# Kernel optimization log

Measured on AMD Instinct MI355X. Metric: run time of the kernel, lower is better.

## Reference

```python
import jax, jax.numpy as jnp
import numpy as np

K1, K2, ALPHA = 0.01, 0.03, 0.84
SIGMA_LEVELS = (1, 2, 4, 7)

def _box_conv(x, k):
    # x: [B,1,H,W]; uniform k x k mean filter, padding k//2 (matches F.conv2d)
    p = k // 2
    w = jnp.ones((1, 1, k, k), x.dtype) / (k * k)
    return jax.lax.conv_general_dilated(
        x, w, window_strides=(1, 1), padding=((p, p), (p, p)),
        dimension_numbers=('NCHW', 'OIHW', 'NCHW'))

def _ssim_mean(X, Y, C1, C2, k):
    ux = _box_conv(X, k)
    uy = _box_conv(Y, k)
    uxx = _box_conv(X * X, k)
    uyy = _box_conv(Y * Y, k)
    uxy = _box_conv(X * Y, k)
    vx = uxx - ux * ux
    vy = uyy - uy * uy
    vxy = uxy - ux * uy
    A1 = 2 * ux * uy + C1
    A2 = 2 * vxy + C2
    B1 = ux * ux + uy * uy + C1
    B2 = vx + vy + C2
    S = (A1 * A2) / (B1 * B2)
    return jnp.mean(S)

def setup_inputs() -> dict:
    key = jax.random.key(0)
    k1, k2 = jax.random.split(key)
    B, H, W = 128, 384, 384
    X = jax.random.uniform(k1, (B, H, W), dtype=jnp.float32)
    Y = jax.random.uniform(k2, (B, H, W), dtype=jnp.float32)
    data_range = jnp.ones((B,), dtype=jnp.float32)
    return {"X": X, "Y": Y, "data_range": data_range}

def reference(X, Y, data_range):
    X4 = X[:, None, :, :]   # [B,1,H,W]
    Y4 = Y[:, None, :, :]
    dr = data_range[:, None, None, None]  # [B,1,1,1]
    C1 = (K1 * dr) ** 2
    C2 = (K2 * dr) ** 2
    # msssim = product of scalar SSIM means over sigma levels (ones_like * scalars).mean()
    msssim = jnp.float32(1.0)
    for k in SIGMA_LEVELS:
        msssim = msssim * _ssim_mean(X4, Y4, C1, C2, k)
    msssim_loss = 1.0 - msssim
    kM = SIGMA_LEVELS[-1]
    fX = _box_conv(X4, kM)
    fY = _box_conv(Y4, kM)
    l1 = jnp.mean(jnp.abs(fX - fY))
    return ALPHA * msssim_loss + (1.0 - ALPHA) * l1
```

## Files before the change

kernel.cpp:

```cpp
#include <hip/hip_runtime.h>


#define W 384
#define H 384
#define NB 128
#define BAND 48
#define NSTRIPS 4
#define NBLK (NSTRIPS * 2 * NB)

typedef __attribute__((ext_vector_type(2))) float f2;

__device__ __forceinline__ float bp(int addr, float v) {
    return __int_as_float(__builtin_amdgcn_ds_bpermute(addr, __float_as_int(v)));
}

__device__ __forceinline__ f2 f2s(float v) { f2 r; r.x = v; r.y = v; return r; }

__device__ __forceinline__ f2 ssim_pm2(f2 Vp, f2 Vm, f2 Vpp, f2 Vmm,
                                       float k2, float c1k42, float c2k42) {
    const f2 p2 = Vp * Vp;
    const f2 m2 = Vm * Vm;
    const f2 d  = p2 - m2;
    const f2 s  = p2 + m2;
    const f2 dq = Vpp - Vmm;
    const f2 sq = Vpp + Vmm;
    const f2 A1 = d + c1k42;
    const f2 B1 = s + c1k42;
    const f2 A2 = __builtin_elementwise_fma(f2s(k2), dq, -d) + c2k42;
    const f2 B2 = __builtin_elementwise_fma(f2s(k2), sq, -s) + c2k42;
    const f2 num = A1 * A2;
    const f2 den = B1 * B2;
    f2 r;
    r.x = num.x * __builtin_amdgcn_rcpf(den.x);
    r.y = num.y * __builtin_amdgcn_rcpf(den.y);
    return r;
}

__global__ __launch_bounds__(256) void msssim_main(
    const float* __restrict__ X, const float* __restrict__ Y,
    const float* __restrict__ dr, float* __restrict__ part)
{
    const int lane = threadIdx.x & 63;
    const int wv   = threadIdx.x >> 6;
    const int strip= blockIdx.x;
    const int band = blockIdx.y * 4 + wv;
    const int b    = blockIdx.z;

    const int i0 = 112 * strip - 4 + 2 * lane;
    const int i1 = i0 + 1;
    const int R0 = BAND * band;

    const int g1hi  = R0 + 48;
    const int g24hi = (band == 7) ? 385 : R0 + 48;

    const float drb = dr[b];
    const float C1 = (0.01f * drb) * (0.01f * drb);
    const float C2 = (0.03f * drb) * (0.03f * drb);
    const float tC1 = 2.f * C1;
    const float C1_2 = C1 * 32.f,    C2_2 = C2 * 32.f;
    const float C1_4 = C1 * 512.f,   C2_4 = C2 * 512.f;
    const float C1_7 = C1 * 4802.f,  C2_7 = C2 * 4802.f;

    const int lo   = 112 * strip;
    const int hi17 = (lo + 112 < 384) ? lo + 112 : 384;
    const int hi24 = (lo + 112 < 385) ? lo + 112 : 385;
    auto own = [&](int j, int hi) -> float {
        return (j >= lo && j < hi) ? 1.f : 0.f;
    };
    const f2 mk1 = { own(i0,     hi17), own(i1,     hi17) };
    const f2 mk2 = { own(i0 + 1, hi24), own(i1 + 1, hi24) };
    const f2 mk4 = { own(i0 + 2, hi24), own(i1 + 2, hi24) };
    const f2 mk7 = { own(i0 + 3, hi17), own(i1 + 3, hi17) };

    f2 mc;
    mc.x = (i0 >= 0 && i0 < W) ? 1.f : 0.f;
    mc.y = (i1 >= 0 && i1 < W) ? 1.f : 0.f;
    const int cE = i0 < 0 ? 0 : (i0 > W - 2 ? W - 2 : i0);

    const int ba1 = ((lane + 1) & 63) << 2;
    const int ba2 = ((lane + 2) & 63) << 2;
    const int ba3 = ((lane + 3) & 63) << 2;

    const float* __restrict__ Xr = X + (size_t)b * (H * W) + cE;
    const float* __restrict__ Yr = Y + (size_t)b * (H * W) + cE;

    f2 r2[4], r4[3][4], r7[6][4], v4s[4], v7s[4];
#pragma unroll
    for (int q = 0; q < 4; ++q) {
        r2[q] = f2s(0.f);
        r4[0][q] = r4[1][q] = r4[2][q] = f2s(0.f);
#pragma unroll
        for (int a = 0; a < 6; ++a) r7[a][q] = f2s(0.f);
        v4s[q] = f2s(0.f); v7s[q] = f2s(0.f);
    }

    f2 ss1v = f2s(0.f), ss2v = f2s(0.f), ss4v = f2s(0.f),
       ss7v = f2s(0.f), l1v  = f2s(0.f);

    const int u0 = R0 - 3;

    f2 rx[3], ry[3];
    auto loadv = [&](int u, int slot) {
        if (u >= 0 && u < H) {
            rx[slot] = *(const f2*)(Xr + (size_t)u * W);
            ry[slot] = *(const f2*)(Yr + (size_t)u * W);
        } else { rx[slot] = f2s(0.f); ry[slot] = f2s(0.f); }
    };

    f2 sp[3], sm[3];
    float sr[3][12];
    auto stageRow = [&](int ps, int bs) {
        const f2 p = (rx[ps] + ry[ps]) * mc;
        const f2 m = (rx[ps] - ry[ps]) * mc;
        sp[bs] = p; sm[bs] = m;
        sr[bs][0]  = bp(ba1, p.x);  sr[bs][1]  = bp(ba1, p.y);
        sr[bs][2]  = bp(ba2, p.x);  sr[bs][3]  = bp(ba2, p.y);
        sr[bs][4]  = bp(ba3, p.x);  sr[bs][5]  = bp(ba3, p.y);
        sr[bs][6]  = bp(ba1, m.x);  sr[bs][7]  = bp(ba1, m.y);
        sr[bs][8]  = bp(ba2, m.x);  sr[bs][9]  = bp(ba2, m.y);
        sr[bs][10] = bp(ba3, m.x);  sr[bs][11] = bp(ba3, m.y);
    };

    auto hwin = [&](f2 v0, float e2, float e3, float e4, float e5,
                    float e6, float e7, f2& w2, f2& w4, f2& w7) {
        const float w2a = v0.x + v0.y;
        const float w2b = v0.y + e2;
        const float t1  = e2 + e3;
        const float w4a = w2a + t1;
        const float t1b = e3 + e4;
        const float w4b = w2b + t1b;
        const float t2  = e4 + e5;
        const float w7a = (w4a + t2) + e6;
        const float t3  = e5 + e6;
        const float w7b = (w4b + t3) + e7;
        w2.x = w2a; w2.y = w2b;
        w4.x = w4a; w4.y = w4b;
        w7.x = w7a; w7.y = w7b;
    };

    loadv(u0,     0);
    loadv(u0 + 1, 1);
    loadv(u0 + 2, 2);
    stageRow(0, 0);
    stageRow(1, 1);
    loadv(u0 + 3, 0);

    for (int s = 0; s < 54; s += 6) {
#pragma unroll
        for (int ph = 0; ph < 6; ++ph) {
            const int u = u0 + s + ph;

            loadv(u + 4, (ph + 1) % 3);

            const int cb = ph % 3;
            const f2 p0 = sp[cb], m0 = sm[cb];
            const float pa1 = sr[cb][0],  pb1 = sr[cb][1];
            const float pa2 = sr[cb][2],  pb2 = sr[cb][3];
            const float pa3 = sr[cb][4],  pb3 = sr[cb][5];
            const float ma1 = sr[cb][6],  mb1 = sr[cb][7];
            const float ma2 = sr[cb][8],  mb2 = sr[cb][9];
            const float ma3 = sr[cb][10], mb3 = sr[cb][11];

            const f2 pp0 = p0 * p0;
            const f2 mm0 = m0 * m0;

            f2 W2[4], W4[4], W7[4];
            hwin(p0,  pa1, pb1, pa2, pb2, pa3, pb3, W2[0], W4[0], W7[0]);
            hwin(m0,  ma1, mb1, ma2, mb2, ma3, mb3, W2[1], W4[1], W7[1]);
            hwin(pp0, pa1*pa1, pb1*pb1, pa2*pa2, pb2*pb2, pa3*pa3, pb3*pb3,
                 W2[2], W4[2], W7[2]);
            hwin(mm0, ma1*ma1, mb1*mb1, ma2*ma2, mb2*mb2, ma3*ma3, mb3*mb3,
                 W2[3], W4[3], W7[3]);

            f2 V2[4], V4[4], V7[4];
#pragma unroll
            for (int q = 0; q < 4; ++q) {
                V2[q] = W2[q] + r2[q];  r2[q] = W2[q];
                const f2 a4v = W4[q] + v4s[q];
                V4[q] = a4v;  v4s[q] = a4v - r4[2][q];
                r4[2][q] = r4[1][q]; r4[1][q] = r4[0][q]; r4[0][q] = W4[q];
                const f2 a7v = W7[q] + v7s[q];
                V7[q] = a7v;  v7s[q] = a7v - r7[5][q];
                r7[5][q] = r7[4][q]; r7[4][q] = r7[3][q]; r7[3][q] = r7[2][q];
                r7[2][q] = r7[1][q]; r7[1][q] = r7[0][q]; r7[0][q] = W7[q];
            }

            if (u >= R0 && u < g1hi) {
                const f2 num = (pp0 - mm0) + tC1;
                const f2 den = (pp0 + mm0) + tC1;
                f2 s1;
                s1.x = num.x * __builtin_amdgcn_rcpf(den.x);
                s1.y = num.y * __builtin_amdgcn_rcpf(den.y);
                ss1v = __builtin_elementwise_fma(s1, mk1, ss1v);
            }
            if (u >= R0 && u < g24hi) {
                ss2v = __builtin_elementwise_fma(
                    ssim_pm2(V2[0], V2[1], V2[2], V2[3], 4.f, C1_2, C2_2),
                    mk2, ss2v);
            }
            {
                const int i = u - 1;
                if (i >= R0 && i < g24hi) {
                    ss4v = __builtin_elementwise_fma(
                        ssim_pm2(V4[0], V4[1], V4[2], V4[3], 16.f, C1_4, C2_4),
                        mk4, ss4v);
                }
            }
            {
                const int i = u - 3;
                if (i >= R0 && i < g1hi) {
                    ss7v = __builtin_elementwise_fma(
                        ssim_pm2(V7[0], V7[1], V7[2], V7[3], 49.f, C1_7, C2_7),
                        mk7, ss7v);
                    f2 av; av.x = fabsf(V7[1].x); av.y = fabsf(V7[1].y);
                    l1v = __builtin_elementwise_fma(av, mk7, l1v);
                }
            }

            stageRow((ph + 2) % 3, (ph + 2) % 3);
        }
    }

    float ss1 = ss1v.x + ss1v.y;
    float ss2 = ss2v.x + ss2v.y;
    float ss4 = ss4v.x + ss4v.y;
    float ss7 = ss7v.x + ss7v.y;
    float l1  = l1v.x  + l1v.y;
#pragma unroll
    for (int d = 32; d > 0; d >>= 1) {
        ss1 += __shfl_down(ss1, d, 64);
        ss2 += __shfl_down(ss2, d, 64);
        ss4 += __shfl_down(ss4, d, 64);
        ss7 += __shfl_down(ss7, d, 64);
        l1  += __shfl_down(l1,  d, 64);
    }
    __shared__ float sred[4][5];
    if (lane == 0) {
        sred[wv][0] = ss1; sred[wv][1] = ss2; sred[wv][2] = ss4;
        sred[wv][3] = ss7; sred[wv][4] = l1;
    }
    __syncthreads();
    if (threadIdx.x == 0) {
        const int bid = ((int)blockIdx.z * 2 + (int)blockIdx.y) * NSTRIPS + (int)blockIdx.x;
#pragma unroll
        for (int q = 0; q < 5; ++q)
            part[bid * 5 + q] = sred[0][q] + sred[1][q] + sred[2][q] + sred[3][q];
    }
}

__global__ __launch_bounds__(256) void reduce_final(
    const float* __restrict__ part, float* __restrict__ out)
{
    const int lane = threadIdx.x & 63;
    const int wv   = threadIdx.x >> 6;
    double d[5] = {0, 0, 0, 0, 0};
    for (int i = threadIdx.x; i < NBLK; i += 256) {
#pragma unroll
        for (int q = 0; q < 5; ++q) d[q] += (double)part[i * 5 + q];
    }
#pragma unroll
    for (int s = 32; s > 0; s >>= 1) {
#pragma unroll
        for (int q = 0; q < 5; ++q) d[q] += __shfl_down(d[q], s, 64);
    }
    __shared__ double sd[4][5];
    if (lane == 0) {
#pragma unroll
        for (int q = 0; q < 5; ++q) sd[wv][q] = d[q];
    }
    __syncthreads();
    if (threadIdx.x == 0) {
        double a[5];
#pragma unroll
        for (int q = 0; q < 5; ++q)
            a[q] = sd[0][q] + sd[1][q] + sd[2][q] + sd[3][q];
        const double n384 = (double)NB * 384.0 * 384.0;
        const double n385 = (double)NB * 385.0 * 385.0;
        const double m  = (a[0] / n384) * (a[1] / n385) * (a[2] / n385) * (a[3] / n384);
        const double l1 = a[4] / 49.0 / n384;
        out[0] = (float)(0.84 * (1.0 - m) + 0.16 * l1);
    }
}

extern "C" void kernel_launch(void* const* d_in, const int* in_sizes, int n_in,
                              void* d_out, int out_size, void* d_ws, size_t ws_size,
                              hipStream_t stream) {
    const float* X  = (const float*)d_in[0];
    const float* Y  = (const float*)d_in[1];
    const float* dr = (const float*)d_in[2];
    float* out  = (float*)d_out;
    float* part = (float*)d_ws;

    dim3 grid(NSTRIPS, 2, NB);
    msssim_main<<<grid, 256, 0, stream>>>(X, Y, dr, part);
    reduce_final<<<1, 256, 0, stream>>>(part, out);
}
```

Before: 201.1 us.

## Remap SIMD pair lanes to two row bands with one column per lane

Each lane now owns a single column, and its two packed SIMD slots hold the same column at rows u and u+192, where before they held two adjacent columns. Horizontal windows therefore need six cross-lane bpermute shifts per value, but the window sums become pure packed-f2 arithmetic with no scalar mixing. The launch changes from 256-thread blocks over 4 strips x 2 groups to 64-thread single-wave blocks on a 7x4 tile grid, which removes the LDS block reduction and syncthreads. In exchange the halo overhead grows, since each wave computes 56 useful columns out of 64, and global loads become scalar per-lane gathers instead of f2 loads.

```diff
diff --git a/kernel.cpp b/kernel.cpp
--- a/kernel.cpp
+++ b/kernel.cpp
@@ -4,16 +4,15 @@
 #define W 384
 #define H 384
 #define NB 128
-#define BAND 48
-#define NSTRIPS 4
-#define NBLK (NSTRIPS * 2 * NB)
+#define NTILES 7
+#define NPAIRS 4
+#define NBLK (NTILES * NPAIRS * NB)
 
 typedef __attribute__((ext_vector_type(2))) float f2;
 
 __device__ __forceinline__ float bp(int addr, float v) {
     return __int_as_float(__builtin_amdgcn_ds_bpermute(addr, __float_as_int(v)));
 }
-
 __device__ __forceinline__ f2 f2s(float v) { f2 r; r.x = v; r.y = v; return r; }
 
 __device__ __forceinline__ f2 ssim_pm2(f2 Vp, f2 Vm, f2 Vpp, f2 Vmm,
@@ -36,22 +35,17 @@
     return r;
 }
 
-__global__ __launch_bounds__(256) void msssim_main(
+__global__ __launch_bounds__(64, 2) void msssim_main(
     const float* __restrict__ X, const float* __restrict__ Y,
     const float* __restrict__ dr, float* __restrict__ part)
 {
-    const int lane = threadIdx.x & 63;
-    const int wv   = threadIdx.x >> 6;
-    const int strip= blockIdx.x;
-    const int band = blockIdx.y * 4 + wv;
+    const int lane = threadIdx.x;
+    const int tile = blockIdx.x;
+    const int g    = blockIdx.y;
     const int b    = blockIdx.z;
 
-    const int i0 = 112 * strip - 4 + 2 * lane;
-    const int i1 = i0 + 1;
-    const int R0 = BAND * band;
-
-    const int g1hi  = R0 + 48;
-    const int g24hi = (band == 7) ? 385 : R0 + 48;
+    const int c  = -3 + 56 * tile + lane;
+    const int R0 = 48 * g;
 
     const float drb = dr[b];
     const float C1 = (0.01f * drb) * (0.01f * drb);
@@ -61,28 +55,25 @@
     const float C1_4 = C1 * 512.f,   C2_4 = C2 * 512.f;
     const float C1_7 = C1 * 4802.f,  C2_7 = C2 * 4802.f;
 
-    const int lo   = 112 * strip;
-    const int hi17 = (lo + 112 < 384) ? lo + 112 : 384;
-    const int hi24 = (lo + 112 < 385) ? lo + 112 : 385;
-    auto own = [&](int j, int hi) -> float {
-        return (j >= lo && j < hi) ? 1.f : 0.f;
-    };
-    const f2 mk1 = { own(i0,     hi17), own(i1,     hi17) };
-    const f2 mk2 = { own(i0 + 1, hi24), own(i1 + 1, hi24) };
-    const f2 mk4 = { own(i0 + 2, hi24), own(i1 + 2, hi24) };
-    const f2 mk7 = { own(i0 + 3, hi17), own(i1 + 3, hi17) };
-
-    f2 mc;
-    mc.x = (i0 >= 0 && i0 < W) ? 1.f : 0.f;
-    mc.y = (i1 >= 0 && i1 < W) ? 1.f : 0.f;
-    const int cE = i0 < 0 ? 0 : (i0 > W - 2 ? W - 2 : i0);
-
-    const int ba1 = ((lane + 1) & 63) << 2;
-    const int ba2 = ((lane + 2) & 63) << 2;
-    const int ba3 = ((lane + 3) & 63) << 2;
-
-    const float* __restrict__ Xr = X + (size_t)b * (H * W) + cE;
-    const float* __restrict__ Yr = Y + (size_t)b * (H * W) + cE;
+    const float m1 = (lane >= 3 && lane <= 58 && c     <= 383) ? 1.f : 0.f;
+    const float m2 = (lane >= 2 && lane <= 57 && c + 1 <= 384) ? 1.f : 0.f;
+    const float m4 = (lane >= 1 && lane <= 56 && c + 2 <= 384) ? 1.f : 0.f;
+    const float m7 = (             lane <= 55 && c + 3 <= 383) ? 1.f : 0.f;
+    const f2 mk1 = f2s(m1);
+    const f2 mk7 = f2s(m7);
+
+    const int k2hi = (g == 3) ? 52 : 51;
+    const int k4hi = (g == 3) ? 53 : 52;
+
+    const float mcol = (c >= 0 && c < W) ? 1.f : 0.f;
+    const int   cc   = c < 0 ? 0 : (c > W - 1 ? W - 1 : c);
+
+    int ad[6];
+#pragma unroll
+    for (int d = 1; d <= 6; ++d) ad[d - 1] = ((lane + d) & 63) << 2;
+
+    const float* __restrict__ Xb = X + (size_t)b * (H * W);
+    const float* __restrict__ Yb = Y + (size_t)b * (H * W);
 
     f2 r2[4], r4[3][4], r7[6][4], v4s[4], v7s[4];
 #pragma unroll
@@ -101,41 +92,32 @@
 
     f2 rx[3], ry[3];
     auto loadv = [&](int u, int slot) {
-        if (u >= 0 && u < H) {
-            rx[slot] = *(const f2*)(Xr + (size_t)u * W);
-            ry[slot] = *(const f2*)(Yr + (size_t)u * W);
-        } else { rx[slot] = f2s(0.f); ry[slot] = f2s(0.f); }
+        float x0 = 0.f, y0 = 0.f, x1 = 0.f, y1 = 0.f;
+        if (u >= 0) {
+            x0 = Xb[(size_t)u * W + cc];
+            y0 = Yb[(size_t)u * W + cc];
+        }
+        const int r1 = u + 192;
+        if (r1 < H) {
+            x1 = Xb[(size_t)r1 * W + cc];
+            y1 = Yb[(size_t)r1 * W + cc];
+        }
+        f2 vx; vx.x = x0; vx.y = x1;
+        f2 vy; vy.x = y0; vy.y = y1;
+        rx[slot] = vx; ry[slot] = vy;
     };
 
-    f2 sp[3], sm[3];
-    float sr[3][12];
-    auto stageRow = [&](int ps, int bs) {
-        const f2 p = (rx[ps] + ry[ps]) * mc;
-        const f2 m = (rx[ps] - ry[ps]) * mc;
-        sp[bs] = p; sm[bs] = m;
-        sr[bs][0]  = bp(ba1, p.x);  sr[bs][1]  = bp(ba1, p.y);
-        sr[bs][2]  = bp(ba2, p.x);  sr[bs][3]  = bp(ba2, p.y);
-        sr[bs][4]  = bp(ba3, p.x);  sr[bs][5]  = bp(ba3, p.y);
-        sr[bs][6]  = bp(ba1, m.x);  sr[bs][7]  = bp(ba1, m.y);
-        sr[bs][8]  = bp(ba2, m.x);  sr[bs][9]  = bp(ba2, m.y);
-        sr[bs][10] = bp(ba3, m.x);  sr[bs][11] = bp(ba3, m.y);
-    };
-
-    auto hwin = [&](f2 v0, float e2, float e3, float e4, float e5,
-                    float e6, float e7, f2& w2, f2& w4, f2& w7) {
-        const float w2a = v0.x + v0.y;
-        const float w2b = v0.y + e2;
-        const float t1  = e2 + e3;
-        const float w4a = w2a + t1;
-        const float t1b = e3 + e4;
-        const float w4b = w2b + t1b;
-        const float t2  = e4 + e5;
-        const float w7a = (w4a + t2) + e6;
-        const float t3  = e5 + e6;
-        const float w7b = (w4b + t3) + e7;
-        w2.x = w2a; w2.y = w2b;
-        w4.x = w4a; w4.y = w4b;
-        w7.x = w7a; w7.y = w7b;
+    f2 sp[3], sm[3], SRp[3][6], SRm[3][6];
+    auto stageRow = [&](int slot, int buf) {
+        const f2 p = (rx[slot] + ry[slot]) * f2s(mcol);
+        const f2 m = (rx[slot] - ry[slot]) * f2s(mcol);
+        sp[buf] = p; sm[buf] = m;
+#pragma unroll
+        for (int d = 0; d < 6; ++d) {
+            f2 tp; tp.x = bp(ad[d], p.x); tp.y = bp(ad[d], p.y);
+            f2 tm; tm.x = bp(ad[d], m.x); tm.y = bp(ad[d], m.y);
+            SRp[buf][d] = tp; SRm[buf][d] = tm;
+        }
     };
 
     loadv(u0,     0);
@@ -143,34 +125,42 @@
     loadv(u0 + 2, 2);
     stageRow(0, 0);
     stageRow(1, 1);
-    loadv(u0 + 3, 0);
 
     for (int s = 0; s < 54; s += 6) {
 #pragma unroll
         for (int ph = 0; ph < 6; ++ph) {
-            const int u = u0 + s + ph;
-
-            loadv(u + 4, (ph + 1) % 3);
+            const int t = s + ph;
+            const int u = u0 + t;
+
+            loadv(u + 3, ph % 3);
 
             const int cb = ph % 3;
             const f2 p0 = sp[cb], m0 = sm[cb];
-            const float pa1 = sr[cb][0],  pb1 = sr[cb][1];
-            const float pa2 = sr[cb][2],  pb2 = sr[cb][3];
-            const float pa3 = sr[cb][4],  pb3 = sr[cb][5];
-            const float ma1 = sr[cb][6],  mb1 = sr[cb][7];
-            const float ma2 = sr[cb][8],  mb2 = sr[cb][9];
-            const float ma3 = sr[cb][10], mb3 = sr[cb][11];
-
-            const f2 pp0 = p0 * p0;
-            const f2 mm0 = m0 * m0;
+            const f2 pp0 = p0 * p0, mm0 = m0 * m0;
 
             f2 W2[4], W4[4], W7[4];
-            hwin(p0,  pa1, pb1, pa2, pb2, pa3, pb3, W2[0], W4[0], W7[0]);
-            hwin(m0,  ma1, mb1, ma2, mb2, ma3, mb3, W2[1], W4[1], W7[1]);
-            hwin(pp0, pa1*pa1, pb1*pb1, pa2*pa2, pb2*pb2, pa3*pa3, pb3*pb3,
-                 W2[2], W4[2], W7[2]);
-            hwin(mm0, ma1*ma1, mb1*mb1, ma2*ma2, mb2*mb2, ma3*ma3, mb3*mb3,
-                 W2[3], W4[3], W7[3]);
+            {
+                const f2 e1 = SRp[cb][0], e2 = SRp[cb][1], e3 = SRp[cb][2];
+                const f2 e4 = SRp[cb][3], e5 = SRp[cb][4], e6 = SRp[cb][5];
+                const f2 f1 = SRm[cb][0], f2e = SRm[cb][1], f3 = SRm[cb][2];
+                const f2 f4 = SRm[cb][3], f5 = SRm[cb][4], f6 = SRm[cb][5];
+                W2[0] = p0 + e1;
+                W4[0] = W2[0] + (e2 + e3);
+                W7[0] = (W4[0] + (e4 + e5)) + e6;
+                W2[1] = m0 + f1;
+                W4[1] = W2[1] + (f2e + f3);
+                W7[1] = (W4[1] + (f4 + f5)) + f6;
+                const f2 s1 = e1 * e1, s2 = e2 * e2, s3 = e3 * e3;
+                const f2 s4 = e4 * e4, s5 = e5 * e5, s6 = e6 * e6;
+                W2[2] = pp0 + s1;
+                W4[2] = W2[2] + (s2 + s3);
+                W7[2] = (W4[2] + (s4 + s5)) + s6;
+                const f2 t1 = f1 * f1, t2 = f2e * f2e, t3 = f3 * f3;
+                const f2 t4 = f4 * f4, t5 = f5 * f5, t6 = f6 * f6;
+                W2[3] = mm0 + t1;
+                W4[3] = W2[3] + (t2 + t3);
+                W7[3] = (W4[3] + (t4 + t5)) + t6;
+            }
 
             f2 V2[4], V4[4], V7[4];
 #pragma unroll
@@ -185,36 +175,32 @@
                 r7[2][q] = r7[1][q]; r7[1][q] = r7[0][q]; r7[0][q] = W7[q];
             }
 
-            if (u >= R0 && u < g1hi) {
+            if (t >= 3 && t < 51) {
                 const f2 num = (pp0 - mm0) + tC1;
                 const f2 den = (pp0 + mm0) + tC1;
-                f2 s1;
-                s1.x = num.x * __builtin_amdgcn_rcpf(den.x);
-                s1.y = num.y * __builtin_amdgcn_rcpf(den.y);
-                ss1v = __builtin_elementwise_fma(s1, mk1, ss1v);
-            }
-            if (u >= R0 && u < g24hi) {
+                f2 s1v;
+                s1v.x = num.x * __builtin_amdgcn_rcpf(den.x);
+                s1v.y = num.y * __builtin_amdgcn_rcpf(den.y);
+                ss1v = __builtin_elementwise_fma(s1v, mk1, ss1v);
+            }
+            if (t >= 3 && t < k2hi) {
+                f2 msk; msk.x = (t < 51) ? m2 : 0.f; msk.y = m2;
                 ss2v = __builtin_elementwise_fma(
                     ssim_pm2(V2[0], V2[1], V2[2], V2[3], 4.f, C1_2, C2_2),
-                    mk2, ss2v);
-            }
-            {
-                const int i = u - 1;
-                if (i >= R0 && i < g24hi) {
-                    ss4v = __builtin_elementwise_fma(
-                        ssim_pm2(V4[0], V4[1], V4[2], V4[3], 16.f, C1_4, C2_4),
-                        mk4, ss4v);
-                }
-            }
-            {
-                const int i = u - 3;
-                if (i >= R0 && i < g1hi) {
-                    ss7v = __builtin_elementwise_fma(
-                        ssim_pm2(V7[0], V7[1], V7[2], V7[3], 49.f, C1_7, C2_7),
-                        mk7, ss7v);
-                    f2 av; av.x = fabsf(V7[1].x); av.y = fabsf(V7[1].y);
-                    l1v = __builtin_elementwise_fma(av, mk7, l1v);
-                }
+                    msk, ss2v);
+            }
+            if (t >= 4 && t < k4hi) {
+                f2 msk; msk.x = (t < 52) ? m4 : 0.f; msk.y = m4;
+                ss4v = __builtin_elementwise_fma(
+                    ssim_pm2(V4[0], V4[1], V4[2], V4[3], 16.f, C1_4, C2_4),
+                    msk, ss4v);
+            }
+            if (t >= 6) {
+                ss7v = __builtin_elementwise_fma(
+                    ssim_pm2(V7[0], V7[1], V7[2], V7[3], 49.f, C1_7, C2_7),
+                    mk7, ss7v);
+                f2 av; av.x = fabsf(V7[1].x); av.y = fabsf(V7[1].y);
+                l1v = __builtin_elementwise_fma(av, mk7, l1v);
             }
 
             stageRow((ph + 2) % 3, (ph + 2) % 3);
@@ -234,17 +220,14 @@
         ss7 += __shfl_down(ss7, d, 64);
         l1  += __shfl_down(l1,  d, 64);
     }
-    __shared__ float sred[4][5];
     if (lane == 0) {
-        sred[wv][0] = ss1; sred[wv][1] = ss2; sred[wv][2] = ss4;
-        sred[wv][3] = ss7; sred[wv][4] = l1;
-    }
-    __syncthreads();
-    if (threadIdx.x == 0) {
-        const int bid = ((int)blockIdx.z * 2 + (int)blockIdx.y) * NSTRIPS + (int)blockIdx.x;
-#pragma unroll
-        for (int q = 0; q < 5; ++q)
-            part[bid * 5 + q] = sred[0][q] + sred[1][q] + sred[2][q] + sred[3][q];
+        const int bid = ((int)blockIdx.z * NPAIRS + (int)blockIdx.y) * NTILES
+                        + (int)blockIdx.x;
+        part[bid * 5 + 0] = ss1;
+        part[bid * 5 + 1] = ss2;
+        part[bid * 5 + 2] = ss4;
+        part[bid * 5 + 3] = ss7;
+        part[bid * 5 + 4] = l1;
     }
 }
 
@@ -291,7 +274,7 @@
     float* out  = (float*)d_out;
     float* part = (float*)d_ws;
 
-    dim3 grid(NSTRIPS, 2, NB);
-    msssim_main<<<grid, 256, 0, stream>>>(X, Y, dr, part);
+    dim3 grid(NTILES, NPAIRS, NB);
+    msssim_main<<<grid, 64, 0, stream>>>(X, Y, dr, part);
     reduce_final<<<1, 256, 0, stream>>>(part, out);
 }
```

Result: slower. 212.5 us (+5.6%).
